# Kernel optimization log

Measured on AMD Instinct MI355X. Metric: run time of the kernel, lower is better.

Reference implementation:

```python
import jax, jax.numpy as jnp
import numpy as np

T_, N_, DIN, D, HEADS, WW, E_, DPE = 8, 20000, 128, 128, 4, 4, 320000, 8
DH = D // HEADS
NEG = -1e30
EPS_GATE = 1e-6


def setup_inputs() -> dict:
    key = jax.random.key(0)
    ks = jax.random.split(key, 10)
    return {
        "H_tilde": jax.random.normal(ks[0], (T_, N_, DIN), jnp.float32),
        "S": jax.random.uniform(ks[1], (T_, N_), jnp.float32),
        "Wq": jax.random.normal(ks[2], (D, DIN), jnp.float32) * 0.05,
        "Wkh": jax.random.normal(ks[3], (D, DIN), jnp.float32) * 0.05,
        "Wkpe": jax.random.normal(ks[4], (D, DPE), jnp.float32) * 0.05,
        "Wv": jax.random.normal(ks[5], (D, DIN), jnp.float32) * 0.05,
        "pe_table": jax.random.normal(ks[6], (WW + 1, DPE), jnp.float32),
        "rel_bias": jax.random.normal(ks[7], (WW + 1,), jnp.float32),
        "src": jax.random.randint(ks[8], (E_,), 0, N_),
        "dst": jax.random.randint(ks[9], (E_,), 0, N_),
    }


def reference(H_tilde, S, Wq, Wkh, Wkpe, Wv, pe_table, rel_bias, src, dst):
    T, N, _ = H_tilde.shape
    H, dh, W = HEADS, DH, WW
    scale = dh ** -0.5
    dtype = H_tilde.dtype

    # Projections (torch Linear: x @ W.T). W_k over concat([H, pe]) splits additively.
    Q = (H_tilde @ Wq.T).reshape(T, N, H, dh)
    K0 = (H_tilde @ Wkh.T).reshape(T, N, H, dh)
    V = (H_tilde @ Wv.T).reshape(T, N, H, dh)
    pe_k = (pe_table @ Wkpe.T).reshape(W + 1, H, dh)
    gate = jnp.log(jnp.clip(S, 0.0, 1.0) + EPS_GATE)  # (T, N)

    # Pad W zero-steps in front so a length-(W+1) slice at t covers t-W..t.
    pad = lambda x: jnp.concatenate([jnp.zeros((W,) + x.shape[1:], x.dtype), x], axis=0)
    Kp, Vp, gp = pad(K0), pad(V), pad(gate)

    def step(_, tq):
        t, Qt = tq  # Qt: (N, H, dh)
        Kwin = jax.lax.dynamic_slice_in_dim(Kp, t, W + 1, 0)[::-1]  # (W+1,N,H,dh), dt=0..W
        Vwin = jax.lax.dynamic_slice_in_dim(Vp, t, W + 1, 0)[::-1]
        gwin = jax.lax.dynamic_slice_in_dim(gp, t, W + 1, 0)[::-1]  # (W+1, N)
        Qd = Qt[dst]  # (E, H, dh)

        scores = []
        for dt in range(W + 1):
            Ks = Kwin[dt][src] + pe_k[dt][None]  # (E, H, dh)
            s = (jnp.einsum('ehc,ehc->eh', Qd, Ks) * scale
                 + rel_bias[dt] + gwin[dt][src][:, None])
            scores.append(jnp.where(dt <= t, s, NEG))  # mask dt > t (W_eff = min(W, t))
        sc = jnp.stack(scores)  # (W+1, E, H)

        # Segment softmax over incoming edges of each dst node, jointly over dt.
        mx = jax.ops.segment_max(sc.transpose(1, 0, 2), dst, num_segments=N)  # (N,W+1,H)
        mx = mx.max(axis=1)  # (N, H)
        valid = (jnp.arange(W + 1) <= t)[:, None, None]
        ex = jnp.where(valid, jnp.exp(sc - mx[dst][None]), 0.0)  # (W+1, E, H)

        denom = jax.ops.segment_sum(ex.sum(axis=0), dst, num_segments=N)  # (N, H)
        numer = jnp.zeros((N, H, dh), dtype)
        for dt in range(W + 1):
            contrib = ex[dt][:, :, None] * Vwin[dt][src]  # (E, H, dh)
            numer = numer + jax.ops.segment_sum(contrib, dst, num_segments=N)

        msg = numer / jnp.maximum(denom, 1e-12)[:, :, None]  # (N, H, dh)
        return None, msg.reshape(N, H * dh)

    _, M_out = jax.lax.scan(step, None, (jnp.arange(T), Q))
    return M_out  # (T, N, d)
```

## Files before the change

### kernel.cpp

```cpp
#include <hip/hip_runtime.h>

typedef unsigned short u16;
typedef unsigned int u32;
typedef __attribute__((ext_vector_type(8))) __bf16 bf16x8;
typedef __attribute__((ext_vector_type(4))) float f32x4;
typedef __attribute__((ext_vector_type(4))) _Float16 f16x4;

constexpr int TT = 8, NN = 20000, DD = 128, EE = 320000;
constexpr int MAXDEG = 64;
constexpr float SCL = 0.17677669529663687f;
constexpr int VSTR = 132;

__device__ __forceinline__ u16 f2bf(float f) {
  u32 u = __float_as_uint(f);
  return (u16)((u + 0x7fffu + ((u >> 16) & 1u)) >> 16);
}
__device__ __forceinline__ u16 f2h(float f) {
  _Float16 h = (_Float16)f;
  return __builtin_bit_cast(unsigned short, h);
}
__device__ __forceinline__ float blo(u32 u) { return __uint_as_float(u << 16); }
__device__ __forceinline__ float bhi(u32 u) { return __uint_as_float(u & 0xffff0000u); }

__global__ void k_zero(int* cnt) {
  int i = blockIdx.x * 256 + threadIdx.x;
  if (i < NN) cnt[i] = 0;
}

__global__ void k_build(const int* __restrict__ src, const int* __restrict__ dst,
                        int* __restrict__ cnt, int* __restrict__ eslot) {
  int i = blockIdx.x * 256 + threadIdx.x;
  if (i < EE) {
    int d = dst[i];
    int p = atomicAdd(&cnt[d], 1);
    if (p < MAXDEG) eslot[d * MAXDEG + p] = src[i];
  }
}

__global__ void k_pek(const float* __restrict__ pe_table, const float* __restrict__ Wkpe,
                      float* __restrict__ pek) {
  int tid = threadIdx.x;
  if (tid < 5 * DD) {
    int dt = tid >> 7, j = tid & 127;
    float s = 0.f;
    for (int p = 0; p < 8; ++p) s += pe_table[dt * 8 + p] * Wkpe[j * 8 + p];
    pek[tid] = s;
  }
}

__global__ __launch_bounds__(256) void k_proj(
    const float* __restrict__ Hm, const float* __restrict__ Wq,
    const float* __restrict__ Wkh, const float* __restrict__ Wv,
    u16* __restrict__ Qb, u16* __restrict__ Kb, u16* __restrict__ Vb) {
  __shared__ u16 As[128 * 128];
  __shared__ u16 Bs[128 * 128];
  const float* Wsel = (blockIdx.y == 0) ? Wq : (blockIdx.y == 1) ? Wkh : Wv;
  u16* Out = (blockIdx.y == 0) ? Qb : (blockIdx.y == 1) ? Kb : Vb;
  const bool asF16 = (blockIdx.y == 2);
  int tid = threadIdx.x;
  size_t m0 = (size_t)blockIdx.x * 128;

  for (int it = 0; it < 8; ++it) {
    int q = it * 256 + tid;
    int r = q >> 4, cb = q & 15;
    int sidx = r * 128 + ((cb ^ (r & 7)) << 3);
    {
      const float* gp = Hm + (m0 + (size_t)r) * DD + cb * 8;
      float4 f0 = *(const float4*)gp;
      float4 f1 = *(const float4*)(gp + 4);
      u16 tmp[8] = {f2bf(f0.x), f2bf(f0.y), f2bf(f0.z), f2bf(f0.w),
                    f2bf(f1.x), f2bf(f1.y), f2bf(f1.z), f2bf(f1.w)};
      *(bf16x8*)(As + sidx) = *(const bf16x8*)tmp;
    }
    {
      const float* wp = Wsel + (size_t)r * DD + cb * 8;
      float4 f0 = *(const float4*)wp;
      float4 f1 = *(const float4*)(wp + 4);
      u16 tmp[8] = {f2bf(f0.x), f2bf(f0.y), f2bf(f0.z), f2bf(f0.w),
                    f2bf(f1.x), f2bf(f1.y), f2bf(f1.z), f2bf(f1.w)};
      *(bf16x8*)(Bs + sidx) = *(const bf16x8*)tmp;
    }
  }
  __syncthreads();

  int lane = tid & 63, wv = tid >> 6;
  int wr = wv >> 1, wc = wv & 1;
  int l15 = lane & 15, lq = lane >> 4;

  f32x4 acc[4][4];
  for (int i = 0; i < 4; ++i)
    for (int j = 0; j < 4; ++j) acc[i][j] = (f32x4){0.f, 0.f, 0.f, 0.f};

  for (int ks = 0; ks < 4; ++ks) {
    bf16x8 a[4], b[4];
    int cb = ks * 4 + lq;
    for (int i = 0; i < 4; ++i) {
      int r = wr * 64 + i * 16 + l15;
      a[i] = *(const bf16x8*)(As + r * 128 + ((cb ^ (r & 7)) << 3));
    }
    for (int j = 0; j < 4; ++j) {
      int r = wc * 64 + j * 16 + l15;
      b[j] = *(const bf16x8*)(Bs + r * 128 + ((cb ^ (r & 7)) << 3));
    }
    for (int i = 0; i < 4; ++i)
      for (int j = 0; j < 4; ++j)
        acc[i][j] = __builtin_amdgcn_mfma_f32_16x16x32_bf16(a[i], b[j], acc[i][j], 0, 0, 0);
  }

  for (int i = 0; i < 4; ++i)
    for (int j = 0; j < 4; ++j)
      for (int g = 0; g < 4; ++g) {
        size_t row = m0 + wr * 64 + i * 16 + lq * 4 + g;
        int col = wc * 64 + j * 16 + l15;
        Out[row * DD + col] = asF16 ? f2h(acc[i][j][g]) : f2bf(acc[i][j][g]);
      }
}

__global__ __launch_bounds__(256) void k_etab(const u16* __restrict__ Qb,
                                              const float* __restrict__ pek,
                                              const float* __restrict__ relb,
                                              float* __restrict__ Etab) {
  int t = blockIdx.y;
  int n = blockIdx.x * 64 + (threadIdx.x >> 2);
  int h = threadIdx.x & 3;
  if (n >= NN) return;
  const u16* qp = Qb + ((size_t)t * NN + n) * DD + h * 32;
  float q[32];
#pragma unroll
  for (int u = 0; u < 4; ++u) {
    uint4 qv = *(const uint4*)(qp + u * 8);
    q[u*8+0]=blo(qv.x); q[u*8+1]=bhi(qv.x); q[u*8+2]=blo(qv.y); q[u*8+3]=bhi(qv.y);
    q[u*8+4]=blo(qv.z); q[u*8+5]=bhi(qv.z); q[u*8+6]=blo(qv.w); q[u*8+7]=bhi(qv.w);
  }
#pragma unroll
  for (int d = 0; d < 5; ++d) {
    float s = 0.f;
#pragma unroll
    for (int c = 0; c < 32; ++c) s += q[c] * pek[d * DD + h * 32 + c];
    Etab[((size_t)(t * 5 + d) * NN + n) * 4 + h] = __expf(s * SCL + relb[d]);
  }
}

__global__ __launch_bounds__(256, 3) void k_agg3(
    const u16* __restrict__ Qb, const u16* __restrict__ Kb, const u16* __restrict__ Vb,
    const float* __restrict__ Sarr, const float* __restrict__ Etab,
    const int* __restrict__ cnt, const int* __restrict__ eslot,
    float* __restrict__ outp) {
  __shared__ int srcS[4][MAXDEG];
  __shared__ float eS[4][40][4];
  __shared__ u16 VldsS[4][2120];
  int tid = threadIdx.x;
  int wv = tid >> 6, lane = tid & 63;
  int n0 = blockIdx.x * 4;
  const int n = n0 + wv;

  for (int i = tid; i < 640; i += 256) {
    int p = i >> 4, nn = (i >> 2) & 3, hh = i & 3;
    eS[nn][p][hh] = Etab[((size_t)p * NN + (n0 + nn)) * 4 + hh];
  }
  int deg = min(cnt[n], MAXDEG);
  srcS[wv][lane] = (lane < deg) ? eslot[n * MAXDEG + lane] : 0;
  __syncthreads();

  const int t16 = lane & 15;
  const int qo = lane >> 4;
  const int qo4 = qo * 4;
  const int degm1 = (deg > 0) ? deg - 1 : 0;
  u16* vw = VldsS[wv];

  uint4 qb[4];
  {
    bool qok = t16 < 8;
    const u16* Qp = Qb + ((size_t)(t16 & 7) * NN + n) * DD + qo * 8;
#pragma unroll
    for (int h = 0; h < 4; ++h) {
      uint4 v = *(const uint4*)(Qp + h * 32);
      qb[h] = qok ? v : make_uint4(0u, 0u, 0u, 0u);
    }
  }

  f32x4 numer[4][2];
#pragma unroll
  for (int h = 0; h < 4; ++h) {
    numer[h][0] = (f32x4){0.f, 0.f, 0.f, 0.f};
    numer[h][1] = (f32x4){0.f, 0.f, 0.f, 0.f};
  }
  float dd[4] = {0.f, 0.f, 0.f, 0.f};

  for (int tp = 0; tp < TT; ++tp) {
    const u16* Ksl = Kb + (size_t)tp * NN * DD;
    const u16* Vsl = Vb + (size_t)tp * NN * DD;
    const float* Ssl = Sarr + (size_t)tp * NN;
    int dt = t16 - tp;
    bool tval = (dt >= 0) && (dt <= 4) && (t16 < 8);
    float Ef[4];
#pragma unroll
    for (int h = 0; h < 4; ++h)
      Ef[h] = tval ? eS[wv][t16 * 5 + dt][h] : 0.f;

    for (int c16 = 0; c16 < deg; c16 += 16) {
      int sA = srcS[wv][min(c16 + t16, degm1)];
      const u16* Kp = Ksl + (size_t)sA * DD + qo * 8;
      uint4 ka0 = *(const uint4*)(Kp);
      uint4 ka1 = *(const uint4*)(Kp + 32);
      uint4 ka2 = *(const uint4*)(Kp + 64);
      uint4 ka3 = *(const uint4*)(Kp + 96);

#pragma unroll
      for (int p = 0; p < 4; ++p) {
        int g = p * 64 + lane;
        int rowg = g >> 4, cg = g & 15;
        int sV = srcS[wv][min(c16 + rowg, degm1)];
        uint4 vv = *(const uint4*)(Vsl + (size_t)sV * DD + cg * 8);
        *(uint2*)(vw + rowg * VSTR + cg * 8) = make_uint2(vv.x, vv.y);
        *(uint2*)(vw + rowg * VSTR + cg * 8 + 4) = make_uint2(vv.z, vv.w);
      }

      float sgv = 0.f;
      if (lane < 16) {
        float s = Ssl[srcS[wv][min(c16 + lane, degm1)]];
        sgv = fminf(fmaxf(s, 0.f), 1.f) + 1e-6f;
      }

      f32x4 z = (f32x4){0.f, 0.f, 0.f, 0.f};
      f32x4 sc[4];
      sc[0] = __builtin_amdgcn_mfma_f32_16x16x32_bf16(
          __builtin_bit_cast(bf16x8, ka0), __builtin_bit_cast(bf16x8, qb[0]), z, 0, 0, 0);
      sc[1] = __builtin_amdgcn_mfma_f32_16x16x32_bf16(
          __builtin_bit_cast(bf16x8, ka1), __builtin_bit_cast(bf16x8, qb[1]), z, 0, 0, 0);
      sc[2] = __builtin_amdgcn_mfma_f32_16x16x32_bf16(
          __builtin_bit_cast(bf16x8, ka2), __builtin_bit_cast(bf16x8, qb[2]), z, 0, 0, 0);
      sc[3] = __builtin_amdgcn_mfma_f32_16x16x32_bf16(
          __builtin_bit_cast(bf16x8, ka3), __builtin_bit_cast(bf16x8, qb[3]), z, 0, 0, 0);

      f16x4 wf[4];
#pragma unroll
      for (int h = 0; h < 4; ++h) {
#pragma unroll
        for (int r = 0; r < 4; ++r) {
          bool kvld = (c16 + qo4 + r) < deg;
          float sgr = __shfl(sgv, qo4 + r);
          float w = __expf(sc[h][r] * SCL) * Ef[h] * (kvld ? sgr : 0.f);
          dd[h] += w;
          wf[h][r] = (_Float16)w;
        }
      }

#pragma unroll
      for (int h = 0; h < 4; ++h) {
#pragma unroll
        for (int tile = 0; tile < 2; ++tile) {
          int choff = h * 32 + tile * 16 + t16;
          ushort4 vr;
          vr.x = vw[(qo4 + 0) * VSTR + choff];
          vr.y = vw[(qo4 + 1) * VSTR + choff];
          vr.z = vw[(qo4 + 2) * VSTR + choff];
          vr.w = vw[(qo4 + 3) * VSTR + choff];
          numer[h][tile] = __builtin_amdgcn_mfma_f32_16x16x16f16(
              wf[h], __builtin_bit_cast(f16x4, vr), numer[h][tile], 0, 0, 0);
        }
      }
    }
  }

#pragma unroll
  for (int h = 0; h < 4; ++h) {
    float Dh = dd[h];
    Dh += __shfl_xor(Dh, 16);
    Dh += __shfl_xor(Dh, 32);
#pragma unroll
    for (int r = 0; r < 4; ++r) {
      int t = qo4 + r;
      float Dt = __shfl(Dh, t);
      if (t < 8) {
        float inv = 1.f / fmaxf(Dt, 1e-12f);
        float* op = outp + ((size_t)t * NN + n) * DD + h * 32;
        op[t16] = numer[h][0][r] * inv;
        op[16 + t16] = numer[h][1][r] * inv;
      }
    }
  }
}

extern "C" void kernel_launch(void* const* d_in, const int* in_sizes, int n_in,
                              void* d_out, int out_size, void* d_ws, size_t ws_size,
                              hipStream_t stream) {
  const float* Hm = (const float*)d_in[0];
  const float* S = (const float*)d_in[1];
  const float* Wq = (const float*)d_in[2];
  const float* Wkh = (const float*)d_in[3];
  const float* Wkpe = (const float*)d_in[4];
  const float* Wv = (const float*)d_in[5];
  const float* pe_table = (const float*)d_in[6];
  const float* relb = (const float*)d_in[7];
  const int* src = (const int*)d_in[8];
  const int* dst = (const int*)d_in[9];
  float* out = (float*)d_out;

  auto aup = [](size_t x) { return (x + 255) & ~(size_t)255; };
  char* base = (char*)d_ws;
  size_t off = 0;
  u16* Qb = (u16*)(base + off); off = aup(off + (size_t)TT * NN * DD * 2);
  u16* Kb = (u16*)(base + off); off = aup(off + (size_t)TT * NN * DD * 2);
  u16* Vb = (u16*)(base + off); off = aup(off + (size_t)TT * NN * DD * 2);
  float* pek = (float*)(base + off); off = aup(off + (size_t)5 * DD * 4);
  float* Etab = (float*)(base + off); off = aup(off + (size_t)TT * 5 * NN * 4 * 4);
  int* cnt = (int*)(base + off); off = aup(off + (size_t)NN * 4);
  int* eslot = (int*)(base + off); off = aup(off + (size_t)NN * MAXDEG * 4);
  (void)ws_size; (void)in_sizes; (void)n_in; (void)out_size;

  k_zero<<<(NN + 255) / 256, 256, 0, stream>>>(cnt);
  k_build<<<(EE + 255) / 256, 256, 0, stream>>>(src, dst, cnt, eslot);
  k_pek<<<1, 640, 0, stream>>>(pe_table, Wkpe, pek);
  k_proj<<<dim3(1250, 3), 256, 0, stream>>>(Hm, Wq, Wkh, Wv, Qb, Kb, Vb);
  k_etab<<<dim3((NN + 63) / 64, TT), 256, 0, stream>>>(Qb, pek, relb, Etab);
  k_agg3<<<NN / 4, 256, 0, stream>>>(Qb, Kb, Vb, S, Etab, cnt, eslot, out);
}
```

Baseline: 356.0 us.

## Software-pipeline gathers in aggregation, use LDS transpose reads, fuse projection and init kernels

```diff
diff --git a/kernel.cpp b/kernel.cpp
--- a/kernel.cpp
+++ b/kernel.cpp
@@ -5,11 +5,12 @@
 typedef __attribute__((ext_vector_type(8))) __bf16 bf16x8;
 typedef __attribute__((ext_vector_type(4))) float f32x4;
 typedef __attribute__((ext_vector_type(4))) _Float16 f16x4;
+typedef __attribute__((ext_vector_type(2))) unsigned u32x2;
 
 constexpr int TT = 8, NN = 20000, DD = 128, EE = 320000;
 constexpr int MAXDEG = 64;
 constexpr float SCL = 0.17677669529663687f;
-constexpr int VSTR = 132;
+constexpr int VBLK = 272;
 
 __device__ __forceinline__ u16 f2bf(float f) {
   u32 u = __float_as_uint(f);
@@ -22,9 +23,16 @@
 __device__ __forceinline__ float blo(u32 u) { return __uint_as_float(u << 16); }
 __device__ __forceinline__ float bhi(u32 u) { return __uint_as_float(u & 0xffff0000u); }
 
-__global__ void k_zero(int* cnt) {
+__global__ void k_init(const float* __restrict__ pe_table, const float* __restrict__ Wkpe,
+                       float* __restrict__ pek, int* __restrict__ cnt) {
   int i = blockIdx.x * 256 + threadIdx.x;
   if (i < NN) cnt[i] = 0;
+  if (i < 5 * DD) {
+    int dt = i >> 7, j = i & 127;
+    float s = 0.f;
+    for (int p = 0; p < 8; ++p) s += pe_table[dt * 8 + p] * Wkpe[j * 8 + p];
+    pek[i] = s;
+  }
 }
 
 __global__ void k_build(const int* __restrict__ src, const int* __restrict__ dst,
@@ -37,26 +45,12 @@
   }
 }
 
-__global__ void k_pek(const float* __restrict__ pe_table, const float* __restrict__ Wkpe,
-                      float* __restrict__ pek) {
-  int tid = threadIdx.x;
-  if (tid < 5 * DD) {
-    int dt = tid >> 7, j = tid & 127;
-    float s = 0.f;
-    for (int p = 0; p < 8; ++p) s += pe_table[dt * 8 + p] * Wkpe[j * 8 + p];
-    pek[tid] = s;
-  }
-}
-
-__global__ __launch_bounds__(256) void k_proj(
+__global__ __launch_bounds__(256) void k_proj3(
     const float* __restrict__ Hm, const float* __restrict__ Wq,
     const float* __restrict__ Wkh, const float* __restrict__ Wv,
     u16* __restrict__ Qb, u16* __restrict__ Kb, u16* __restrict__ Vb) {
   __shared__ u16 As[128 * 128];
   __shared__ u16 Bs[128 * 128];
-  const float* Wsel = (blockIdx.y == 0) ? Wq : (blockIdx.y == 1) ? Wkh : Wv;
-  u16* Out = (blockIdx.y == 0) ? Qb : (blockIdx.y == 1) ? Kb : Vb;
-  const bool asF16 = (blockIdx.y == 2);
   int tid = threadIdx.x;
   size_t m0 = (size_t)blockIdx.x * 128;
 
@@ -64,15 +58,27 @@
     int q = it * 256 + tid;
     int r = q >> 4, cb = q & 15;
     int sidx = r * 128 + ((cb ^ (r & 7)) << 3);
-    {
-      const float* gp = Hm + (m0 + (size_t)r) * DD + cb * 8;
-      float4 f0 = *(const float4*)gp;
-      float4 f1 = *(const float4*)(gp + 4);
-      u16 tmp[8] = {f2bf(f0.x), f2bf(f0.y), f2bf(f0.z), f2bf(f0.w),
-                    f2bf(f1.x), f2bf(f1.y), f2bf(f1.z), f2bf(f1.w)};
-      *(bf16x8*)(As + sidx) = *(const bf16x8*)tmp;
-    }
-    {
+    const float* gp = Hm + (m0 + (size_t)r) * DD + cb * 8;
+    float4 f0 = *(const float4*)gp;
+    float4 f1 = *(const float4*)(gp + 4);
+    u16 tmp[8] = {f2bf(f0.x), f2bf(f0.y), f2bf(f0.z), f2bf(f0.w),
+                  f2bf(f1.x), f2bf(f1.y), f2bf(f1.z), f2bf(f1.w)};
+    *(bf16x8*)(As + sidx) = *(const bf16x8*)tmp;
+  }
+
+  int lane = tid & 63, wv = tid >> 6;
+  int wr = wv >> 1, wc = wv & 1;
+  int l15 = lane & 15, lq = lane >> 4;
+
+  for (int y = 0; y < 3; ++y) {
+    const float* Wsel = (y == 0) ? Wq : (y == 1) ? Wkh : Wv;
+    u16* Out = (y == 0) ? Qb : (y == 1) ? Kb : Vb;
+    const bool asF16 = (y == 2);
+    __syncthreads();
+    for (int it = 0; it < 8; ++it) {
+      int q = it * 256 + tid;
+      int r = q >> 4, cb = q & 15;
+      int sidx = r * 128 + ((cb ^ (r & 7)) << 3);
       const float* wp = Wsel + (size_t)r * DD + cb * 8;
       float4 f0 = *(const float4*)wp;
       float4 f1 = *(const float4*)(wp + 4);
@@ -80,40 +86,36 @@
                     f2bf(f1.x), f2bf(f1.y), f2bf(f1.z), f2bf(f1.w)};
       *(bf16x8*)(Bs + sidx) = *(const bf16x8*)tmp;
     }
-  }
-  __syncthreads();
-
-  int lane = tid & 63, wv = tid >> 6;
-  int wr = wv >> 1, wc = wv & 1;
-  int l15 = lane & 15, lq = lane >> 4;
-
-  f32x4 acc[4][4];
-  for (int i = 0; i < 4; ++i)
-    for (int j = 0; j < 4; ++j) acc[i][j] = (f32x4){0.f, 0.f, 0.f, 0.f};
-
-  for (int ks = 0; ks < 4; ++ks) {
-    bf16x8 a[4], b[4];
-    int cb = ks * 4 + lq;
-    for (int i = 0; i < 4; ++i) {
-      int r = wr * 64 + i * 16 + l15;
-      a[i] = *(const bf16x8*)(As + r * 128 + ((cb ^ (r & 7)) << 3));
-    }
-    for (int j = 0; j < 4; ++j) {
-      int r = wc * 64 + j * 16 + l15;
-      b[j] = *(const bf16x8*)(Bs + r * 128 + ((cb ^ (r & 7)) << 3));
-    }
+    __syncthreads();
+
+    f32x4 acc[4][4];
+    for (int i = 0; i < 4; ++i)
+      for (int j = 0; j < 4; ++j) acc[i][j] = (f32x4){0.f, 0.f, 0.f, 0.f};
+
+    for (int ks = 0; ks < 4; ++ks) {
+      bf16x8 a[4], b[4];
+      int cb = ks * 4 + lq;
+      for (int i = 0; i < 4; ++i) {
+        int r = wr * 64 + i * 16 + l15;
+        a[i] = *(const bf16x8*)(As + r * 128 + ((cb ^ (r & 7)) << 3));
+      }
+      for (int j = 0; j < 4; ++j) {
+        int r = wc * 64 + j * 16 + l15;
+        b[j] = *(const bf16x8*)(Bs + r * 128 + ((cb ^ (r & 7)) << 3));
+      }
+      for (int i = 0; i < 4; ++i)
+        for (int j = 0; j < 4; ++j)
+          acc[i][j] = __builtin_amdgcn_mfma_f32_16x16x32_bf16(a[i], b[j], acc[i][j], 0, 0, 0);
+    }
+
     for (int i = 0; i < 4; ++i)
       for (int j = 0; j < 4; ++j)
-        acc[i][j] = __builtin_amdgcn_mfma_f32_16x16x32_bf16(a[i], b[j], acc[i][j], 0, 0, 0);
-  }
-
-  for (int i = 0; i < 4; ++i)
-    for (int j = 0; j < 4; ++j)
-      for (int g = 0; g < 4; ++g) {
-        size_t row = m0 + wr * 64 + i * 16 + lq * 4 + g;
-        int col = wc * 64 + j * 16 + l15;
-        Out[row * DD + col] = asF16 ? f2h(acc[i][j][g]) : f2bf(acc[i][j][g]);
-      }
+        for (int g = 0; g < 4; ++g) {
+          size_t row = m0 + wr * 64 + i * 16 + lq * 4 + g;
+          int col = wc * 64 + j * 16 + l15;
+          Out[row * DD + col] = asF16 ? f2h(acc[i][j][g]) : f2bf(acc[i][j][g]);
+        }
+  }
 }
 
 __global__ __launch_bounds__(256) void k_etab(const u16* __restrict__ Qb,
@@ -141,14 +143,14 @@
   }
 }
 
-__global__ __launch_bounds__(256, 3) void k_agg3(
+__global__ __launch_bounds__(256, 3) void k_agg4(
     const u16* __restrict__ Qb, const u16* __restrict__ Kb, const u16* __restrict__ Vb,
     const float* __restrict__ Sarr, const float* __restrict__ Etab,
     const int* __restrict__ cnt, const int* __restrict__ eslot,
     float* __restrict__ outp) {
   __shared__ int srcS[4][MAXDEG];
   __shared__ float eS[4][40][4];
-  __shared__ u16 VldsS[4][2120];
+  __shared__ u16 VldsS[4][8 * VBLK];
   int tid = threadIdx.x;
   int wv = tid >> 6, lane = tid & 63;
   int n0 = blockIdx.x * 4;
@@ -162,11 +164,7 @@
   srcS[wv][lane] = (lane < deg) ? eslot[n * MAXDEG + lane] : 0;
   __syncthreads();
 
-  const int t16 = lane & 15;
-  const int qo = lane >> 4;
-  const int qo4 = qo * 4;
-  const int degm1 = (deg > 0) ? deg - 1 : 0;
-  u16* vw = VldsS[wv];
+  const int t16 = lane & 15, qo = lane >> 4, qo4 = qo * 4;
 
   uint4 qb[4];
   {
@@ -187,79 +185,120 @@
   }
   float dd[4] = {0.f, 0.f, 0.f, 0.f};
 
-  for (int tp = 0; tp < TT; ++tp) {
-    const u16* Ksl = Kb + (size_t)tp * NN * DD;
-    const u16* Vsl = Vb + (size_t)tp * NN * DD;
-    const float* Ssl = Sarr + (size_t)tp * NN;
-    int dt = t16 - tp;
-    bool tval = (dt >= 0) && (dt <= 4) && (t16 < 8);
-    float Ef[4];
-#pragma unroll
-    for (int h = 0; h < 4; ++h)
-      Ef[h] = tval ? eS[wv][t16 * 5 + dt][h] : 0.f;
-
-    for (int c16 = 0; c16 < deg; c16 += 16) {
+  if (deg > 0) {
+    const int degm1 = deg - 1;
+    const int nch = (deg + 15) >> 4;
+    const int cmax = nch << 4;
+    const int nj = nch * 8;
+
+    u16* vbuf = &VldsS[wv][0];
+    unsigned vb0 = (unsigned)(uintptr_t)vbuf;
+    unsigned trbase = vb0 + lane * 8;
+    unsigned wbase = ((unsigned)((lane & 15) >> 1)) * (VBLK * 2) + qo * 32 + (lane & 1) * 16;
+
+    uint4 kaA[4], kaB[4], vvB[4];
+    float sgA = 0.f, sgB = 0.f;
+
+    auto issue = [&](int tp, int c16, uint4 ka[4], uint4 vvn[4], float& sgn) {
+      const u16* Ksl = Kb + (size_t)tp * (NN * DD);
+      const u16* Vsl = Vb + (size_t)tp * (NN * DD);
       int sA = srcS[wv][min(c16 + t16, degm1)];
       const u16* Kp = Ksl + (size_t)sA * DD + qo * 8;
-      uint4 ka0 = *(const uint4*)(Kp);
-      uint4 ka1 = *(const uint4*)(Kp + 32);
-      uint4 ka2 = *(const uint4*)(Kp + 64);
-      uint4 ka3 = *(const uint4*)(Kp + 96);
-
+      ka[0] = *(const uint4*)(Kp);
+      ka[1] = *(const uint4*)(Kp + 32);
+      ka[2] = *(const uint4*)(Kp + 64);
+      ka[3] = *(const uint4*)(Kp + 96);
 #pragma unroll
       for (int p = 0; p < 4; ++p) {
-        int g = p * 64 + lane;
-        int rowg = g >> 4, cg = g & 15;
+        int rowg = p * 4 + qo;
         int sV = srcS[wv][min(c16 + rowg, degm1)];
-        uint4 vv = *(const uint4*)(Vsl + (size_t)sV * DD + cg * 8);
-        *(uint2*)(vw + rowg * VSTR + cg * 8) = make_uint2(vv.x, vv.y);
-        *(uint2*)(vw + rowg * VSTR + cg * 8 + 4) = make_uint2(vv.z, vv.w);
-      }
-
-      float sgv = 0.f;
+        vvn[p] = *(const uint4*)(Vsl + (size_t)sV * DD + (lane & 15) * 8);
+      }
+      sgn = 0.f;
       if (lane < 16) {
-        float s = Ssl[srcS[wv][min(c16 + lane, degm1)]];
-        sgv = fminf(fmaxf(s, 0.f), 1.f) + 1e-6f;
-      }
+        float s = Sarr[(size_t)tp * NN + srcS[wv][min(c16 + lane, degm1)]];
+        sgn = fminf(fmaxf(s, 0.f), 1.f) + 1e-6f;
+      }
+    };
+
+    auto writeV = [&](uint4 vvn[4]) {
+#pragma unroll
+      for (int p = 0; p < 4; ++p)
+        *(uint4*)((char*)vbuf + (wbase + p * 128)) = vvn[p];
+    };
+
+    auto compute = [&](uint4 ka[4], float sg, int tp, int c16) {
+      int dt = t16 - tp;
+      bool tval = (dt >= 0) && (dt <= 4) && (t16 < 8);
+      float Ef[4];
+#pragma unroll
+      for (int h = 0; h < 4; ++h)
+        Ef[h] = tval ? eS[wv][t16 * 5 + dt][h] : 0.f;
 
       f32x4 z = (f32x4){0.f, 0.f, 0.f, 0.f};
       f32x4 sc[4];
-      sc[0] = __builtin_amdgcn_mfma_f32_16x16x32_bf16(
-          __builtin_bit_cast(bf16x8, ka0), __builtin_bit_cast(bf16x8, qb[0]), z, 0, 0, 0);
-      sc[1] = __builtin_amdgcn_mfma_f32_16x16x32_bf16(
-          __builtin_bit_cast(bf16x8, ka1), __builtin_bit_cast(bf16x8, qb[1]), z, 0, 0, 0);
-      sc[2] = __builtin_amdgcn_mfma_f32_16x16x32_bf16(
-          __builtin_bit_cast(bf16x8, ka2), __builtin_bit_cast(bf16x8, qb[2]), z, 0, 0, 0);
-      sc[3] = __builtin_amdgcn_mfma_f32_16x16x32_bf16(
-          __builtin_bit_cast(bf16x8, ka3), __builtin_bit_cast(bf16x8, qb[3]), z, 0, 0, 0);
-
+#pragma unroll
+      for (int h = 0; h < 4; ++h)
+        sc[h] = __builtin_amdgcn_mfma_f32_16x16x32_bf16(
+            __builtin_bit_cast(bf16x8, ka[h]), __builtin_bit_cast(bf16x8, qb[h]), z, 0, 0, 0);
+
+      float sgm[4];
+#pragma unroll
+      for (int r = 0; r < 4; ++r) {
+        float sgr = __shfl(sg, qo4 + r);
+        sgm[r] = ((c16 + qo4 + r) < deg) ? sgr : 0.f;
+      }
       f16x4 wf[4];
 #pragma unroll
       for (int h = 0; h < 4; ++h) {
 #pragma unroll
         for (int r = 0; r < 4; ++r) {
-          bool kvld = (c16 + qo4 + r) < deg;
-          float sgr = __shfl(sgv, qo4 + r);
-          float w = __expf(sc[h][r] * SCL) * Ef[h] * (kvld ? sgr : 0.f);
+          float w = __expf(sc[h][r] * SCL) * Ef[h] * sgm[r];
           dd[h] += w;
           wf[h][r] = (_Float16)w;
         }
       }
 
+      __builtin_amdgcn_sched_barrier(0);
+      u32x2 vr[4][2];
 #pragma unroll
       for (int h = 0; h < 4; ++h) {
 #pragma unroll
         for (int tile = 0; tile < 2; ++tile) {
-          int choff = h * 32 + tile * 16 + t16;
-          ushort4 vr;
-          vr.x = vw[(qo4 + 0) * VSTR + choff];
-          vr.y = vw[(qo4 + 1) * VSTR + choff];
-          vr.z = vw[(qo4 + 2) * VSTR + choff];
-          vr.w = vw[(qo4 + 3) * VSTR + choff];
+          unsigned a = trbase + (unsigned)(h * 2 + tile) * (VBLK * 2);
+          asm volatile("ds_read_b64_tr_b16 %0, %1" : "=v"(vr[h][tile]) : "v"(a));
+        }
+      }
+      asm volatile("s_waitcnt lgkmcnt(0)");
+      __builtin_amdgcn_sched_barrier(0);
+#pragma unroll
+      for (int h = 0; h < 4; ++h) {
+#pragma unroll
+        for (int tile = 0; tile < 2; ++tile) {
           numer[h][tile] = __builtin_amdgcn_mfma_f32_16x16x16f16(
-              wf[h], __builtin_bit_cast(f16x4, vr), numer[h][tile], 0, 0, 0);
+              wf[h], __builtin_bit_cast(f16x4, vr[h][tile]), numer[h][tile], 0, 0, 0);
         }
       }
+    };
+
+    int tpj = 0, cj = 0;
+    issue(0, 0, kaA, vvB, sgA);
+    writeV(vvB);
+    int tpn = 0, cn = 16;
+    if (cn >= cmax) { cn = 0; tpn = 1; }
+
+    for (int j = 0; j < nj; ++j) {
+      bool more = (j + 1) < nj;
+      if (more) issue(tpn, cn, kaB, vvB, sgB);
+      compute(kaA, sgA, tpj, cj);
+      __builtin_amdgcn_sched_barrier(0);
+      if (more) writeV(vvB);
+#pragma unroll
+      for (int x = 0; x < 4; ++x) kaA[x] = kaB[x];
+      sgA = sgB;
+      tpj = tpn; cj = cn;
+      cn += 16;
+      if (cn >= cmax) { cn = 0; ++tpn; }
     }
   }
 
@@ -309,10 +348,9 @@
   int* eslot = (int*)(base + off); off = aup(off + (size_t)NN * MAXDEG * 4);
   (void)ws_size; (void)in_sizes; (void)n_in; (void)out_size;
 
-  k_zero<<<(NN + 255) / 256, 256, 0, stream>>>(cnt);
+  k_init<<<(NN + 255) / 256, 256, 0, stream>>>(pe_table, Wkpe, pek, cnt);
   k_build<<<(EE + 255) / 256, 256, 0, stream>>>(src, dst, cnt, eslot);
-  k_pek<<<1, 640, 0, stream>>>(pe_table, Wkpe, pek);
-  k_proj<<<dim3(1250, 3), 256, 0, stream>>>(Hm, Wq, Wkh, Wv, Qb, Kb, Vb);
+  k_proj3<<<1250, 256, 0, stream>>>(Hm, Wq, Wkh, Wv, Qb, Kb, Vb);
   k_etab<<<dim3((NN + 63) / 64, TT), 256, 0, stream>>>(Qb, pek, relb, Etab);
-  k_agg3<<<NN / 4, 256, 0, stream>>>(Qb, Kb, Vb, S, Etab, cnt, eslot, out);
-}
+  k_agg4<<<NN / 4, 256, 0, stream>>>(Qb, Kb, Vb, S, Etab, cnt, eslot, out);
+}
```

Result: slower. 483.8 us (+35.9%).
